# Kernel tuning notes

Hardware: AMD Instinct MI355X
Metric: run time of the kernel (lower is better)

Reference implementation:

```python
import jax, jax.numpy as jnp
import numpy as np

CHANNELS = 512
KSIZE = 5


def conv1d(x, w, b, pad):
    # x: (B, Cin, T), w: (Cout, Cin, k) -> (B, Cout, T)
    y = jax.lax.conv_general_dilated(
        x, w, window_strides=(1,), padding=[(pad, pad)],
        dimension_numbers=('NCH', 'OIH', 'NCH'))
    return y + b[None, :, None]


def setup_inputs() -> dict:
    key = jax.random.key(0)
    ks = jax.random.split(key, 10)
    B, C, T, K = 16, CHANNELS, 2048, KSIZE
    s = 0.02  # conv init scale
    return {
        'x': jax.random.normal(ks[0], (B, C, T), jnp.float32),
        'offset_w': jax.random.normal(ks[1], (2 * K, C, 3), jnp.float32) * s,
        'offset_b': jnp.zeros((2 * K,), jnp.float32),
        'mod_w': jax.random.normal(ks[2], (K, C, 3), jnp.float32) * s,
        'mod_b': jnp.zeros((K,), jnp.float32),
        'weight': jax.random.normal(ks[3], (C, C, K), jnp.float32),
        'rp1_w': jax.random.normal(ks[4], (C // 2, C, 3), jnp.float32) * s,
        'rp1_b': jnp.zeros((C // 2,), jnp.float32),
        'rp2_w': jax.random.normal(ks[5], (1, C // 2, 1), jnp.float32) * s,
        'rp2_b': jnp.zeros((1,), jnp.float32),
    }


def deformable_conv1d(x, offset, modulator, weight):
    B, C, T = x.shape
    K = weight.shape[-1]
    # offset: (B, 2K, T) -> (B, T, 2, K); only component 0 is used (as in torch src)
    off = offset.reshape(B, 2, K, T).transpose(0, 3, 1, 2)[:, :, 0, :]   # (B, T, K)
    mod = modulator.reshape(B, K, T).transpose(0, 2, 1)                   # (B, T, K)
    base = jnp.arange(T, dtype=x.dtype)[None, :, None]
    kpos = (jnp.arange(K, dtype=x.dtype) - K // 2)[None, None, :]
    pos = jnp.clip(base + kpos + off, 0, T - 1)                           # (B, T, K)
    pf = jnp.clip(jnp.floor(pos).astype(jnp.int32), 0, T - 1)
    pc = jnp.clip(jnp.ceil(pos).astype(jnp.int32), 0, T - 1)
    wf = pc.astype(x.dtype) - pos    # NB: both weights are 0 at integer pos (faithful to source)
    wc = pos - pf.astype(x.dtype)
    # gather along time for all channels at once: (B, C, T, K)
    sf = jnp.take_along_axis(x, pf.reshape(B, 1, T * K), axis=2).reshape(B, C, T, K)
    sc = jnp.take_along_axis(x, pc.reshape(B, 1, T * K), axis=2).reshape(B, C, T, K)
    sampled = sf * wf[:, None] + sc * wc[:, None]
    # only diagonal weight[c, c, k] is used in the source loops
    wdiag = weight[jnp.arange(C), jnp.arange(C), :]                       # (C, K)
    return jnp.einsum('bctk,ck,btk->bct', sampled, wdiag, mod)


def reference(x, offset_w, offset_b, mod_w, mod_b, weight, rp1_w, rp1_b, rp2_w, rp2_b):
    offset = conv1d(x, offset_w, offset_b, pad=1)            # (B, 2K, T)
    modulator = jax.nn.sigmoid(conv1d(x, mod_w, mod_b, pad=1))  # (B, K, T)
    deformed = deformable_conv1d(x, offset, modulator, weight)  # (B, C, T)
    h = jax.nn.relu(conv1d(deformed, rp1_w, rp1_b, pad=1))
    strength = conv1d(h, rp2_w, rp2_b, pad=0)[:, 0, :]          # (B, T)
    return deformed, strength
```

## Files before the change

kernel.cpp:

```cpp
#include <hip/hip_runtime.h>
#include <hip/hip_bf16.h>

#define CHN 512
#define TLEN 2048
#define KSZ 5
#define BATCH 16

typedef __hip_bfloat16 bf16;
typedef short bf16x8 __attribute__((ext_vector_type(8)));
typedef float f32x4  __attribute__((ext_vector_type(4)));

#define SAMP_BYTES (BATCH*TLEN*KSZ*8)
#define W1T_BYTES  (983040)
#define W1T_ELEMS  (16*3*256*40)

__global__ __launch_bounds__(256) void kP(const float* __restrict__ w1,
                                          bf16* __restrict__ w1t)
{
  int idx  = blockIdx.x*256 + threadIdx.x;
  int c40  = idx % 40;
  int rest = idx / 40;
  int co   = rest & 255;
  int rr   = rest >> 8;
  int r    = rr % 3;
  int ch   = rr / 3;
  float v = 0.f;
  if (c40 < 32) v = w1[(size_t)co*(CHN*3) + (ch*32 + c40)*3 + r];
  w1t[idx] = __float2bfloat16(v);
}

__global__ __launch_bounds__(256) void kW(const float* __restrict__ ow,
    const float* __restrict__ mw, float* __restrict__ wpk)
{
  int idx = blockIdx.x*256 + threadIdx.x;
  int j = idx & 31, c = idx >> 5;
  float v = 0.f;
  if (j < 15)      { int o = j/3,  d = j - o*3;  v = ow[o*(CHN*3) + c*3 + d]; }
  else if (j < 30) { int jj = j-15; int o = jj/3, d = jj - o*3;
                     v = mw[o*(CHN*3) + c*3 + d]; }
  wpk[idx] = v;
}

__global__ __launch_bounds__(512) void kS(const float* __restrict__ x,
    const float* __restrict__ wpk, const float* __restrict__ ob,
    const float* __restrict__ mb, float2* __restrict__ samp)
{
  int b  = blockIdx.y;
  int t0 = blockIdx.x*64;
  int tx = threadIdx.x;
  int cg = threadIdx.y;
  int t  = t0 + tx;

  __shared__ float red[8][64][10];

  float acc[10];
  #pragma unroll
  for (int i=0;i<10;++i) acc[i]=0.f;
  const float* xb = x + (size_t)b*CHN*TLEN;
  int c0 = cg*64;
  #pragma unroll 4
  for (int c=c0;c<c0+64;++c) {
    int cu = __builtin_amdgcn_readfirstlane(c);
    const float* wp = wpk + cu*32;
    const float* xr = xb + (size_t)cu*TLEN;
    float xm = (t>0)      ? xr[t-1] : 0.f;
    float xc = xr[t];
    float xp = (t<TLEN-1) ? xr[t+1] : 0.f;
    #pragma unroll
    for (int o=0;o<5;++o) {
      acc[o]   = fmaf(xm, wp[o*3+0],    acc[o]);
      acc[o]   = fmaf(xc, wp[o*3+1],    acc[o]);
      acc[o]   = fmaf(xp, wp[o*3+2],    acc[o]);
      acc[5+o] = fmaf(xm, wp[15+o*3+0], acc[5+o]);
      acc[5+o] = fmaf(xc, wp[15+o*3+1], acc[5+o]);
      acc[5+o] = fmaf(xp, wp[15+o*3+2], acc[5+o]);
    }
  }
  #pragma unroll
  for (int i=0;i<10;++i) red[cg][tx][i] = acc[i];
  __syncthreads();
  for (int s=4;s>0;s>>=1) {
    if (cg < s) {
      #pragma unroll
      for (int i=0;i<10;++i) red[cg][tx][i] += red[cg+s][tx][i];
    }
    __syncthreads();
  }
  if (cg==0) {
    #pragma unroll
    for (int k=0;k<KSZ;++k) {
      float off = red[0][tx][k]   + ob[k];
      float mv  = red[0][tx][5+k] + mb[k];
      float sig = 1.f/(1.f + expf(-mv));
      float pos = (float)(t + k - 2) + off;
      pos = fminf(fmaxf(pos, 0.f), (float)(TLEN-1));
      samp[((size_t)b*TLEN + t)*KSZ + k] = make_float2(pos, sig);
    }
  }
}

#define BT   128
#define HALO 16
#define XLEN 160

__global__ __launch_bounds__(256) void kDf(const float* __restrict__ x,
    const float* __restrict__ wgt, const float2* __restrict__ sampg,
    float* __restrict__ out)
{
  int b  = blockIdx.z;
  int c0 = blockIdx.y*64;
  int t0 = blockIdx.x*BT;
  int tx = threadIdx.x, cy = threadIdx.y;
  int tid = cy*64 + tx;

  __shared__ float  xs[64*XLEN];
  __shared__ float2 sp[BT*KSZ];
  __shared__ int okf;

  int lo = min(max(t0 - HALO, 0), TLEN - XLEN);

  if (tid == 0) okf = 1;
  for (int i = tid; i < BT*KSZ; i += 256)
    sp[i] = sampg[((size_t)b*TLEN + t0)*KSZ + i];

  const float* xb = x + (size_t)b*CHN*TLEN;
  #pragma unroll
  for (int it = 0; it < 10; ++it) {
    int idx = tid + it*256;
    int c  = idx / 40;
    int c4 = idx - c*40;
    const float* src = xb + (size_t)(c0 + c)*TLEN + lo + c4*4;
    __builtin_amdgcn_global_load_lds(
        (const __attribute__((address_space(1))) unsigned int*)src,
        (__attribute__((address_space(3))) unsigned int*)&xs[idx*4],
        16, 0, 0);
  }
  __syncthreads();

  int   bl[2][KSZ];
  float wf[2][KSZ], wc[2][KSZ];
  bool ok = true;
  #pragma unroll
  for (int j=0;j<2;++j)
    #pragma unroll
    for (int k=0;k<KSZ;++k) {
      float2 s = sp[(j*64+tx)*KSZ + k];
      float pos = s.x, sig = s.y;
      float pf = floorf(pos), pc = ceilf(pos);
      int base = min((int)pf, TLEN-2);
      wf[j][k] = (pc - pos)*sig;
      wc[j][k] = (pos - pf)*sig;
      int bloc = base - lo;
      bl[j][k] = bloc;
      ok = ok && (bloc >= 0) && (bloc <= XLEN-2);
    }
  if (!ok) okf = 0;
  __syncthreads();
  int fast = okf;

  if (fast) {
    #pragma unroll 2
    for (int i=0;i<16;++i) {
      int cl = cy*16 + i;
      int cu = __builtin_amdgcn_readfirstlane(c0 + cl);
      const float* wd = wgt + (size_t)cu*(CHN*KSZ) + (size_t)cu*KSZ;
      float w0 = wd[0], w1v = wd[1], w2v = wd[2], w3 = wd[3], w4 = wd[4];
      const float* xr = xs + cl*XLEN;
      float o0, o1;
      {
        float a = 0.f;
        a = fmaf(fmaf(xr[bl[0][0]+1], wc[0][0], xr[bl[0][0]]*wf[0][0]), w0,  a);
        a = fmaf(fmaf(xr[bl[0][1]+1], wc[0][1], xr[bl[0][1]]*wf[0][1]), w1v, a);
        a = fmaf(fmaf(xr[bl[0][2]+1], wc[0][2], xr[bl[0][2]]*wf[0][2]), w2v, a);
        a = fmaf(fmaf(xr[bl[0][3]+1], wc[0][3], xr[bl[0][3]]*wf[0][3]), w3,  a);
        a = fmaf(fmaf(xr[bl[0][4]+1], wc[0][4], xr[bl[0][4]]*wf[0][4]), w4,  a);
        o0 = a;
      }
      {
        float a = 0.f;
        a = fmaf(fmaf(xr[bl[1][0]+1], wc[1][0], xr[bl[1][0]]*wf[1][0]), w0,  a);
        a = fmaf(fmaf(xr[bl[1][1]+1], wc[1][1], xr[bl[1][1]]*wf[1][1]), w1v, a);
        a = fmaf(fmaf(xr[bl[1][2]+1], wc[1][2], xr[bl[1][2]]*wf[1][2]), w2v, a);
        a = fmaf(fmaf(xr[bl[1][3]+1], wc[1][3], xr[bl[1][3]]*wf[1][3]), w3,  a);
        a = fmaf(fmaf(xr[bl[1][4]+1], wc[1][4], xr[bl[1][4]]*wf[1][4]), w4,  a);
        o1 = a;
      }
      size_t op = ((size_t)b*CHN + cu)*TLEN + t0 + tx;
      out[op]      = o0;
      out[op + 64] = o1;
    }
  } else {
    for (int i=0;i<16;++i) {
      int cl = cy*16 + i;
      int cu = __builtin_amdgcn_readfirstlane(c0 + cl);
      const float* wd = wgt + (size_t)cu*(CHN*KSZ) + (size_t)cu*KSZ;
      float wk0 = wd[0], wk1 = wd[1], wk2 = wd[2], wk3 = wd[3], wk4 = wd[4];
      const float* xr = xb + (size_t)cu*TLEN + lo;
      float o[2];
      #pragma unroll
      for (int j=0;j<2;++j) {
        float a = 0.f;
        a = fmaf(fmaf(xr[bl[j][0]+1], wc[j][0], xr[bl[j][0]]*wf[j][0]), wk0, a);
        a = fmaf(fmaf(xr[bl[j][1]+1], wc[j][1], xr[bl[j][1]]*wf[j][1]), wk1, a);
        a = fmaf(fmaf(xr[bl[j][2]+1], wc[j][2], xr[bl[j][2]]*wf[j][2]), wk2, a);
        a = fmaf(fmaf(xr[bl[j][3]+1], wc[j][3], xr[bl[j][3]]*wf[j][3]), wk3, a);
        a = fmaf(fmaf(xr[bl[j][4]+1], wc[j][4], xr[bl[j][4]]*wf[j][4]), wk4, a);
        o[j] = a;
      }
      size_t op = ((size_t)b*CHN + cu)*TLEN + t0 + tx;
      out[op]      = o[0];
      out[op + 64] = o[1];
    }
  }
}

__global__ __launch_bounds__(512, 2) void k2(const float* __restrict__ def,
    const bf16* __restrict__ w1t, const float* __restrict__ b1,
    const float* __restrict__ w2, const float* __restrict__ b2p,
    float* __restrict__ outs)
{
  int n0 = blockIdx.x*128;
  int b  = n0 / TLEN;
  int t0 = n0 % TLEN;
  int tid  = threadIdx.x;
  int lane = tid & 63;
  int wave = tid >> 6;
  int wM   = wave & 3;
  int wN   = wave >> 2;
  int ln15 = lane & 15, quad = lane >> 4;

  __shared__ bf16 Ws[3*256*40];
  __shared__ bf16 Dt[130*40];
  __shared__ float Ss[128];

  f32x4 acc[4][4];
  #pragma unroll
  for (int i=0;i<4;++i)
    #pragma unroll
    for (int j=0;j<4;++j) acc[i][j] = (f32x4){0.f,0.f,0.f,0.f};

  for (int ch=0; ch<16; ++ch) {
    const char* gsrc = (const char*)(w1t + (size_t)ch*(3*256*40));
    for (int of = tid*16; of < 61440; of += 8192) {
      __builtin_amdgcn_global_load_lds(
          (const __attribute__((address_space(1))) unsigned int*)(gsrc + of),
          (__attribute__((address_space(3))) unsigned int*)((char*)Ws + of),
          16, 0, 0);
    }
    int ci0 = ch*32;
    #pragma unroll
    for (int j=0;j<9;++j) {
      int idx = tid + j*512;
      if (idx < 4160) {
        int ci = idx / 130, tt = idx - ci*130;
        int t = t0 - 1 + tt;
        float v = (t>=0 && t<TLEN)
            ? def[((size_t)b*CHN + ci0 + ci)*TLEN + t] : 0.f;
        Dt[tt*40 + ci] = __float2bfloat16(v);
      }
    }
    __syncthreads();

    #pragma unroll
    for (int r=0;r<3;++r) {
      bf16x8 af[4], bfr[4];
      #pragma unroll
      for (int mt=0;mt<4;++mt)
        af[mt] = *(const bf16x8*)&Ws[(size_t)(r*256 + wM*64 + mt*16 + ln15)*40 + quad*8];
      #pragma unroll
      for (int nt=0;nt<4;++nt)
        bfr[nt] = *(const bf16x8*)&Dt[(size_t)(wN*64 + nt*16 + ln15 + r)*40 + quad*8];
      #pragma unroll
      for (int mt=0;mt<4;++mt)
        #pragma unroll
        for (int nt=0;nt<4;++nt)
          acc[mt][nt] = __builtin_amdgcn_mfma_f32_16x16x32_bf16(
              af[mt], bfr[nt], acc[mt][nt], 0, 0, 0);
    }
    __syncthreads();
  }

  float part[4] = {0.f,0.f,0.f,0.f};
  #pragma unroll
  for (int mt=0;mt<4;++mt) {
    #pragma unroll
    for (int rr=0;rr<4;++rr) {
      int row = wM*64 + mt*16 + quad*4 + rr;
      float bias = b1[row];
      float wv   = w2[row];
      #pragma unroll
      for (int nt=0;nt<4;++nt) {
        float h = acc[mt][nt][rr] + bias;
        h = fmaxf(h, 0.f);
        part[nt] = fmaf(h, wv, part[nt]);
      }
    }
  }
  if (tid < 128) Ss[tid] = 0.f;
  __syncthreads();
  #pragma unroll
  for (int nt=0;nt<4;++nt)
    atomicAdd(&Ss[wN*64 + nt*16 + ln15], part[nt]);
  __syncthreads();
  if (tid < 128)
    outs[n0 + tid] = Ss[tid] + b2p[0];
}

extern "C" void kernel_launch(void* const* d_in, const int* in_sizes, int n_in,
                              void* d_out, int out_size, void* d_ws, size_t ws_size,
                              hipStream_t stream) {
  const float* x  = (const float*)d_in[0];
  const float* ow = (const float*)d_in[1];
  const float* ob = (const float*)d_in[2];
  const float* mw = (const float*)d_in[3];
  const float* mb = (const float*)d_in[4];
  const float* wg = (const float*)d_in[5];
  const float* w1 = (const float*)d_in[6];
  const float* b1 = (const float*)d_in[7];
  const float* w2 = (const float*)d_in[8];
  const float* b2 = (const float*)d_in[9];

  float* out_def = (float*)d_out;
  float* out_str = out_def + (size_t)BATCH*CHN*TLEN;

  float2* samp = (float2*)d_ws;
  bf16*   w1t  = (bf16*)((char*)d_ws + SAMP_BYTES);
  float*  wpk  = (float*)((char*)d_ws + SAMP_BYTES + W1T_BYTES);

  kP <<<dim3(W1T_ELEMS/256), 256, 0, stream>>>(w1, w1t);
  kW <<<dim3(64), 256, 0, stream>>>(ow, mw, wpk);
  kS <<<dim3(TLEN/64, BATCH), dim3(64,8), 0, stream>>>(x, wpk, ob, mb, samp);
  kDf<<<dim3(TLEN/BT, CHN/64, BATCH), dim3(64,4), 0, stream>>>(x, wg, samp, out_def);
  k2 <<<dim3(BATCH*TLEN/128), 512, 0, stream>>>(out_def, w1t, b1, w2, b2, out_str);
}
```

Before: 251.3 us.

## Split k2 output channels across two blocks and vectorize deformed tile staging

The rp1 GEMM kernel now splits its 256 output channels across two blocks in a second grid dimension. Each block has 256 threads and half the weight tile in LDS. Partial strength sums are combined with global atomicAdd into an output that a new kernel pre-fills with the rp2 bias. Staging of the deformed input tile now has each thread convert 8 channels and write a 16-byte bf16x8 vector to LDS, replacing scalar stores. This doubles block count and cuts LDS per block for occupancy, at the cost of reading the deformed activations twice, using global atomics, and adding an extra launch.

```diff
diff --git a/kernel.cpp b/kernel.cpp
--- a/kernel.cpp
+++ b/kernel.cpp
@@ -39,6 +39,12 @@
   else if (j < 30) { int jj = j-15; int o = jj/3, d = jj - o*3;
                      v = mw[o*(CHN*3) + c*3 + d]; }
   wpk[idx] = v;
+}
+
+__global__ __launch_bounds__(256) void kZ(float* __restrict__ outs,
+                                          const float* __restrict__ b2p)
+{
+  outs[blockIdx.x*256 + threadIdx.x] = b2p[0];
 }
 
 __global__ __launch_bounds__(512) void kS(const float* __restrict__ x,
@@ -214,22 +220,22 @@
   }
 }
 
-__global__ __launch_bounds__(512, 2) void k2(const float* __restrict__ def,
+__global__ __launch_bounds__(256, 2) void k2(const float* __restrict__ def,
     const bf16* __restrict__ w1t, const float* __restrict__ b1,
-    const float* __restrict__ w2, const float* __restrict__ b2p,
-    float* __restrict__ outs)
+    const float* __restrict__ w2, float* __restrict__ outs)
 {
   int n0 = blockIdx.x*128;
+  int m0 = blockIdx.y;
   int b  = n0 / TLEN;
   int t0 = n0 % TLEN;
   int tid  = threadIdx.x;
   int lane = tid & 63;
   int wave = tid >> 6;
-  int wM   = wave & 3;
-  int wN   = wave >> 2;
+  int wM   = wave & 1;
+  int wN   = wave >> 1;
   int ln15 = lane & 15, quad = lane >> 4;
 
-  __shared__ bf16 Ws[3*256*40];
+  __shared__ bf16 Ws[3*128*40];
   __shared__ bf16 Dt[130*40];
   __shared__ float Ss[128];
 
@@ -240,24 +246,33 @@
     for (int j=0;j<4;++j) acc[i][j] = (f32x4){0.f,0.f,0.f,0.f};
 
   for (int ch=0; ch<16; ++ch) {
-    const char* gsrc = (const char*)(w1t + (size_t)ch*(3*256*40));
-    for (int of = tid*16; of < 61440; of += 8192) {
-      __builtin_amdgcn_global_load_lds(
-          (const __attribute__((address_space(1))) unsigned int*)(gsrc + of),
-          (__attribute__((address_space(3))) unsigned int*)((char*)Ws + of),
-          16, 0, 0);
+    #pragma unroll
+    for (int r=0;r<3;++r) {
+      const char* gs = (const char*)(w1t + ((size_t)(ch*3+r)*256 + m0*128)*40);
+      char* ld = (char*)Ws + r*10240;
+      for (int of = tid*16; of < 10240; of += 4096) {
+        __builtin_amdgcn_global_load_lds(
+            (const __attribute__((address_space(1))) unsigned int*)(gs + of),
+            (__attribute__((address_space(3))) unsigned int*)(ld + of),
+            16, 0, 0);
+      }
     }
     int ci0 = ch*32;
-    #pragma unroll
-    for (int j=0;j<9;++j) {
-      int idx = tid + j*512;
-      if (idx < 4160) {
-        int ci = idx / 130, tt = idx - ci*130;
-        int t = t0 - 1 + tt;
-        float v = (t>=0 && t<TLEN)
-            ? def[((size_t)b*CHN + ci0 + ci)*TLEN + t] : 0.f;
-        Dt[tt*40 + ci] = __float2bfloat16(v);
-      }
+    for (int s = tid; s < 520; s += 256) {
+      int g  = s / 130;
+      int tt = s - g*130;
+      int t  = t0 - 1 + tt;
+      bf16x8 v = (bf16x8){0,0,0,0,0,0,0,0};
+      if (t >= 0 && t < TLEN) {
+        const float* dp = def + ((size_t)b*CHN + ci0 + g*8)*TLEN + t;
+        #pragma unroll
+        for (int j=0;j<8;++j) {
+          union { bf16 h; short u; } cv;
+          cv.h = __float2bfloat16(dp[(size_t)j*TLEN]);
+          v[j] = cv.u;
+        }
+      }
+      *(bf16x8*)((char*)Dt + tt*80 + g*16) = v;
     }
     __syncthreads();
 
@@ -266,7 +281,7 @@
       bf16x8 af[4], bfr[4];
       #pragma unroll
       for (int mt=0;mt<4;++mt)
-        af[mt] = *(const bf16x8*)&Ws[(size_t)(r*256 + wM*64 + mt*16 + ln15)*40 + quad*8];
+        af[mt] = *(const bf16x8*)&Ws[(size_t)(r*128 + wM*64 + mt*16 + ln15)*40 + quad*8];
       #pragma unroll
       for (int nt=0;nt<4;++nt)
         bfr[nt] = *(const bf16x8*)&Dt[(size_t)(wN*64 + nt*16 + ln15 + r)*40 + quad*8];
@@ -285,7 +300,7 @@
   for (int mt=0;mt<4;++mt) {
     #pragma unroll
     for (int rr=0;rr<4;++rr) {
-      int row = wM*64 + mt*16 + quad*4 + rr;
+      int row = m0*128 + wM*64 + mt*16 + quad*4 + rr;
       float bias = b1[row];
       float wv   = w2[row];
       #pragma unroll
@@ -303,7 +318,7 @@
     atomicAdd(&Ss[wN*64 + nt*16 + ln15], part[nt]);
   __syncthreads();
   if (tid < 128)
-    outs[n0 + tid] = Ss[tid] + b2p[0];
+    atomicAdd(&outs[n0 + tid], Ss[tid]);
 }
 
 extern "C" void kernel_launch(void* const* d_in, const int* in_sizes, int n_in,
@@ -329,7 +344,8 @@
 
   kP <<<dim3(W1T_ELEMS/256), 256, 0, stream>>>(w1, w1t);
   kW <<<dim3(64), 256, 0, stream>>>(ow, mw, wpk);
+  kZ <<<dim3(BATCH*TLEN/256), 256, 0, stream>>>(out_str, b2);
   kS <<<dim3(TLEN/64, BATCH), dim3(64,8), 0, stream>>>(x, wpk, ob, mb, samp);
   kDf<<<dim3(TLEN/BT, CHN/64, BATCH), dim3(64,4), 0, stream>>>(x, wg, samp, out_def);
-  k2 <<<dim3(BATCH*TLEN/128), 512, 0, stream>>>(out_def, w1t, b1, w2, b2, out_str);
-}
+  k2 <<<dim3(BATCH*TLEN/128, 2), 256, 0, stream>>>(out_def, w1t, b1, w2, out_str);
+}
```

Result: faster. 234.8 us (-6.6%).

## Double-buffer k2 conv, split output channels across blocks, merge prep kernels

Applied to the files above, without the earlier changes.

Rewrites the rp1/rp2 kernel to double-buffer the weight and activation tiles in LDS. The next channel chunk's loads are issued before the current chunk's MFMA work, which removes one barrier per chunk and hides global latency. The block tile changes from 256 output channels by 128 timesteps to 128 channels by 256 timesteps, split over a second grid dimension. Partial strength sums are combined with global atomics, so the bias is pre-written by a merged prep kernel that also replaces the two weight-packing kernels. This adds LDS usage and atomic traffic, and the float summation order becomes nondeterministic.

```diff
diff --git a/kernel.cpp b/kernel.cpp
--- a/kernel.cpp
+++ b/kernel.cpp
@@ -14,31 +14,35 @@
 #define W1T_BYTES  (983040)
 #define W1T_ELEMS  (16*3*256*40)
 
-__global__ __launch_bounds__(256) void kP(const float* __restrict__ w1,
-                                          bf16* __restrict__ w1t)
+__global__ __launch_bounds__(256) void kPrep(const float* __restrict__ w1,
+    bf16* __restrict__ w1t, const float* __restrict__ ow,
+    const float* __restrict__ mw, float* __restrict__ wpk,
+    float* __restrict__ outs, const float* __restrict__ b2p)
 {
-  int idx  = blockIdx.x*256 + threadIdx.x;
-  int c40  = idx % 40;
-  int rest = idx / 40;
-  int co   = rest & 255;
-  int rr   = rest >> 8;
-  int r    = rr % 3;
-  int ch   = rr / 3;
-  float v = 0.f;
-  if (c40 < 32) v = w1[(size_t)co*(CHN*3) + (ch*32 + c40)*3 + r];
-  w1t[idx] = __float2bfloat16(v);
-}
-
-__global__ __launch_bounds__(256) void kW(const float* __restrict__ ow,
-    const float* __restrict__ mw, float* __restrict__ wpk)
-{
-  int idx = blockIdx.x*256 + threadIdx.x;
-  int j = idx & 31, c = idx >> 5;
-  float v = 0.f;
-  if (j < 15)      { int o = j/3,  d = j - o*3;  v = ow[o*(CHN*3) + c*3 + d]; }
-  else if (j < 30) { int jj = j-15; int o = jj/3, d = jj - o*3;
-                     v = mw[o*(CHN*3) + c*3 + d]; }
-  wpk[idx] = v;
+  int bx = blockIdx.x;
+  int tidl = threadIdx.x;
+  if (bx < 1920) {
+    int idx  = bx*256 + tidl;
+    int c40  = idx % 40;
+    int rest = idx / 40;
+    int co   = rest & 255;
+    int rr   = rest >> 8;
+    int r    = rr % 3;
+    int ch   = rr / 3;
+    float v = 0.f;
+    if (c40 < 32) v = w1[(size_t)co*(CHN*3) + (ch*32 + c40)*3 + r];
+    w1t[idx] = __float2bfloat16(v);
+  } else if (bx < 1984) {
+    int idx = (bx-1920)*256 + tidl;
+    int j = idx & 31, c = idx >> 5;
+    float v = 0.f;
+    if (j < 15)      { int o = j/3,  d = j - o*3;  v = ow[o*(CHN*3) + c*3 + d]; }
+    else if (j < 30) { int jj = j-15; int o = jj/3, d = jj - o*3;
+                       v = mw[o*(CHN*3) + c*3 + d]; }
+    wpk[idx] = v;
+  } else {
+    outs[(bx-1984)*256 + tidl] = b2p[0];
+  }
 }
 
 __global__ __launch_bounds__(512) void kS(const float* __restrict__ x,
@@ -214,24 +218,97 @@
   }
 }
 
+#define DMA_WS(dst, ch_) do {                                                  \
+  _Pragma("unroll")                                                            \
+  for (int r=0;r<3;++r) {                                                      \
+    const char* gs = (const char*)(w1t + ((size_t)((ch_)*3+r)*256 + m0*128)*40);\
+    char* ld = (char*)&Ws[dst][0] + r*10240;                                   \
+    int of = tid*16;                                                           \
+    __builtin_amdgcn_global_load_lds(                                          \
+        (const __attribute__((address_space(1))) unsigned int*)(gs+of),        \
+        (__attribute__((address_space(3))) unsigned int*)(ld+of), 16, 0, 0);   \
+    if (tid < 128)                                                             \
+      __builtin_amdgcn_global_load_lds(                                        \
+          (const __attribute__((address_space(1))) unsigned int*)(gs+of+8192), \
+          (__attribute__((address_space(3))) unsigned int*)(ld+of+8192),       \
+          16, 0, 0);                                                           \
+  }                                                                            \
+} while(0)
+
+#define LOAD_DT(ch_) do {                                                      \
+  int ci0 = (ch_)*32;                                                          \
+  const float* dpb = def + ((size_t)b*CHN + ci0 + g*8)*TLEN;                   \
+  int tA = t0 - 1 + tq;                                                        \
+  int tB = tA + 128;                                                           \
+  int tC = tA + 256;                                                           \
+  _Pragma("unroll")                                                            \
+  for (int j=0;j<8;++j) ra[j] = (tA>=0 && tA<TLEN) ? dpb[(size_t)j*TLEN+tA] : 0.f;\
+  _Pragma("unroll")                                                            \
+  for (int j=0;j<8;++j) rb[j] = (tB<TLEN) ? dpb[(size_t)j*TLEN+tB] : 0.f;      \
+  if (tq < 2) {                                                                \
+    _Pragma("unroll")                                                          \
+    for (int j=0;j<8;++j) rc[j] = (tC<TLEN) ? dpb[(size_t)j*TLEN+tC] : 0.f;    \
+  }                                                                            \
+} while(0)
+
+#define WRITE_DT(dst) do {                                                     \
+  bf16x8 v;                                                                    \
+  _Pragma("unroll")                                                            \
+  for (int j=0;j<8;++j) { union{bf16 h; short u;} cv;                          \
+    cv.h = __float2bfloat16(ra[j]); v[j] = cv.u; }                             \
+  *(bf16x8*)((char*)&Dt[dst][0] + tq*80 + g*16) = v;                           \
+  _Pragma("unroll")                                                            \
+  for (int j=0;j<8;++j) { union{bf16 h; short u;} cv;                          \
+    cv.h = __float2bfloat16(rb[j]); v[j] = cv.u; }                             \
+  *(bf16x8*)((char*)&Dt[dst][0] + (tq+128)*80 + g*16) = v;                     \
+  if (tq < 2) {                                                                \
+    _Pragma("unroll")                                                          \
+    for (int j=0;j<8;++j) { union{bf16 h; short u;} cv;                        \
+      cv.h = __float2bfloat16(rc[j]); v[j] = cv.u; }                           \
+    *(bf16x8*)((char*)&Dt[dst][0] + (tq+256)*80 + g*16) = v;                   \
+  }                                                                            \
+} while(0)
+
+#define COMPUTE(cur) do {                                                      \
+  _Pragma("unroll")                                                            \
+  for (int r=0;r<3;++r) {                                                      \
+    bf16x8 af[4], bfr[4];                                                      \
+    _Pragma("unroll")                                                          \
+    for (int mt=0;mt<4;++mt)                                                   \
+      af[mt] = *(const bf16x8*)&Ws[cur][(size_t)(r*128 + wM*64 + mt*16 + ln15)*40 + quad*8];\
+    _Pragma("unroll")                                                          \
+    for (int nt=0;nt<4;++nt)                                                   \
+      bfr[nt] = *(const bf16x8*)&Dt[cur][(size_t)(wN*64 + nt*16 + ln15 + r)*40 + quad*8];\
+    _Pragma("unroll")                                                          \
+    for (int mt=0;mt<4;++mt)                                                   \
+      _Pragma("unroll")                                                        \
+      for (int nt=0;nt<4;++nt)                                                 \
+        acc[mt][nt] = __builtin_amdgcn_mfma_f32_16x16x32_bf16(                 \
+            af[mt], bfr[nt], acc[mt][nt], 0, 0, 0);                            \
+  }                                                                            \
+} while(0)
+
 __global__ __launch_bounds__(512, 2) void k2(const float* __restrict__ def,
     const bf16* __restrict__ w1t, const float* __restrict__ b1,
-    const float* __restrict__ w2, const float* __restrict__ b2p,
-    float* __restrict__ outs)
+    const float* __restrict__ w2, float* __restrict__ outs)
 {
-  int n0 = blockIdx.x*128;
+  int n0 = blockIdx.x*256;
+  int m0 = blockIdx.y;
   int b  = n0 / TLEN;
   int t0 = n0 % TLEN;
   int tid  = threadIdx.x;
   int lane = tid & 63;
   int wave = tid >> 6;
-  int wM   = wave & 3;
-  int wN   = wave >> 2;
+  int wM   = wave & 1;
+  int wN   = wave >> 1;
   int ln15 = lane & 15, quad = lane >> 4;
 
-  __shared__ bf16 Ws[3*256*40];
-  __shared__ bf16 Dt[130*40];
-  __shared__ float Ss[128];
+  __shared__ bf16 Ws[2][3*128*40];
+  __shared__ bf16 Dt[2][258*40];
+  __shared__ float Ss[256];
+
+  int g  = tid >> 7;
+  int tq = tid & 127;
 
   f32x4 acc[4][4];
   #pragma unroll
@@ -239,45 +316,26 @@
     #pragma unroll
     for (int j=0;j<4;++j) acc[i][j] = (f32x4){0.f,0.f,0.f,0.f};
 
+  float ra[8], rb[8], rc[8];
+  #pragma unroll
+  for (int j=0;j<8;++j) rc[j] = 0.f;
+
+  DMA_WS(0, 0);
+  LOAD_DT(0);
+  WRITE_DT(0);
+  __syncthreads();
+
   for (int ch=0; ch<16; ++ch) {
-    const char* gsrc = (const char*)(w1t + (size_t)ch*(3*256*40));
-    for (int of = tid*16; of < 61440; of += 8192) {
-      __builtin_amdgcn_global_load_lds(
-          (const __attribute__((address_space(1))) unsigned int*)(gsrc + of),
-          (__attribute__((address_space(3))) unsigned int*)((char*)Ws + of),
-          16, 0, 0);
-    }
-    int ci0 = ch*32;
-    #pragma unroll
-    for (int j=0;j<9;++j) {
-      int idx = tid + j*512;
-      if (idx < 4160) {
-        int ci = idx / 130, tt = idx - ci*130;
-        int t = t0 - 1 + tt;
-        float v = (t>=0 && t<TLEN)
-            ? def[((size_t)b*CHN + ci0 + ci)*TLEN + t] : 0.f;
-        Dt[tt*40 + ci] = __float2bfloat16(v);
-      }
-    }
+    int cur = ch & 1;
+    int nxt = cur ^ 1;
+    if (ch < 15) {
+      DMA_WS(nxt, ch+1);
+      LOAD_DT(ch+1);
+    }
+    COMPUTE(cur);
+    if (ch < 15)
+      WRITE_DT(nxt);
     __syncthreads();
-
-    #pragma unroll
-    for (int r=0;r<3;++r) {
-      bf16x8 af[4], bfr[4];
-      #pragma unroll
-      for (int mt=0;mt<4;++mt)
-        af[mt] = *(const bf16x8*)&Ws[(size_t)(r*256 + wM*64 + mt*16 + ln15)*40 + quad*8];
-      #pragma unroll
-      for (int nt=0;nt<4;++nt)
-        bfr[nt] = *(const bf16x8*)&Dt[(size_t)(wN*64 + nt*16 + ln15 + r)*40 + quad*8];
-      #pragma unroll
-      for (int mt=0;mt<4;++mt)
-        #pragma unroll
-        for (int nt=0;nt<4;++nt)
-          acc[mt][nt] = __builtin_amdgcn_mfma_f32_16x16x32_bf16(
-              af[mt], bfr[nt], acc[mt][nt], 0, 0, 0);
-    }
-    __syncthreads();
   }
 
   float part[4] = {0.f,0.f,0.f,0.f};
@@ -285,7 +343,7 @@
   for (int mt=0;mt<4;++mt) {
     #pragma unroll
     for (int rr=0;rr<4;++rr) {
-      int row = wM*64 + mt*16 + quad*4 + rr;
+      int row = m0*128 + wM*64 + mt*16 + quad*4 + rr;
       float bias = b1[row];
       float wv   = w2[row];
       #pragma unroll
@@ -296,14 +354,14 @@
       }
     }
   }
-  if (tid < 128) Ss[tid] = 0.f;
+  if (tid < 256) Ss[tid] = 0.f;
   __syncthreads();
   #pragma unroll
   for (int nt=0;nt<4;++nt)
     atomicAdd(&Ss[wN*64 + nt*16 + ln15], part[nt]);
   __syncthreads();
-  if (tid < 128)
-    outs[n0 + tid] = Ss[tid] + b2p[0];
+  if (tid < 256)
+    atomicAdd(&outs[n0 + tid], Ss[tid]);
 }
 
 extern "C" void kernel_launch(void* const* d_in, const int* in_sizes, int n_in,
@@ -327,9 +385,8 @@
   bf16*   w1t  = (bf16*)((char*)d_ws + SAMP_BYTES);
   float*  wpk  = (float*)((char*)d_ws + SAMP_BYTES + W1T_BYTES);
 
-  kP <<<dim3(W1T_ELEMS/256), 256, 0, stream>>>(w1, w1t);
-  kW <<<dim3(64), 256, 0, stream>>>(ow, mw, wpk);
-  kS <<<dim3(TLEN/64, BATCH), dim3(64,8), 0, stream>>>(x, wpk, ob, mb, samp);
-  kDf<<<dim3(TLEN/BT, CHN/64, BATCH), dim3(64,4), 0, stream>>>(x, wg, samp, out_def);
-  k2 <<<dim3(BATCH*TLEN/128), 512, 0, stream>>>(out_def, w1t, b1, w2, b2, out_str);
-}
+  kPrep<<<dim3(1920+64+128), 256, 0, stream>>>(w1, w1t, ow, mw, wpk, out_str, b2);
+  kS   <<<dim3(TLEN/64, BATCH), dim3(64,8), 0, stream>>>(x, wpk, ob, mb, samp);
+  kDf  <<<dim3(TLEN/BT, CHN/64, BATCH), dim3(64,4), 0, stream>>>(x, wg, samp, out_def);
+  k2   <<<dim3(BATCH*TLEN/256, 2), 512, 0, stream>>>(out_def, w1t, b1, w2, out_str);
+}
```

Result: slower. 279.9 us (+11.4%).
